# Performance work log

Hardware: AMD Instinct MI355X
Metric: run time of the kernel (lower is better)

## Reference

```python
import jax, jax.numpy as jnp
import numpy as np

B, S, D, H = 8, 1024, 1024, 16
HD = D // H  # head dim 64
NUM_REL = 7


def setup_inputs() -> dict:
    key = jax.random.key(0)
    ks = jax.random.split(key, 10)
    s = 0.02
    return {
        "hidden_states": jax.random.normal(ks[0], (B, S, D), dtype=jnp.float32),
        "attention_mask": jnp.zeros((B, 1, 1, S), dtype=jnp.float32),
        "relation": jax.random.randint(ks[1], (B, S, S), 0, NUM_REL, dtype=jnp.int32),
        "Wq": jax.random.normal(ks[2], (D, D), dtype=jnp.float32) * s,
        "bq": jnp.zeros((D,), dtype=jnp.float32),
        "Wk": jax.random.normal(ks[3], (D, D), dtype=jnp.float32) * s,
        "bk": jnp.zeros((D,), dtype=jnp.float32),
        "Wv": jax.random.normal(ks[4], (D, D), dtype=jnp.float32) * s,
        "bv": jnp.zeros((D,), dtype=jnp.float32),
        "rel_emb": jax.random.normal(ks[5], (NUM_REL, H), dtype=jnp.float32) * s,
    }


def reference(hidden_states, attention_mask, relation, Wq, bq, Wk, bk, Wv, bv, rel_emb):
    def heads(x):  # [B,S,D] -> [B,H,S,HD]
        return x.reshape(B, S, H, HD).transpose(0, 2, 1, 3)

    q = heads(hidden_states @ Wq.T + bq)
    k = heads(hidden_states @ Wk.T + bk)
    v = heads(hidden_states @ Wv.T + bv)

    scores = jnp.einsum("bhqd,bhkd->bhqk", q, k) / jnp.sqrt(jnp.float32(HD))
    # relation bias: gather [B,S,S,H] then move H to dim 1
    rel_bias = rel_emb[relation].transpose(0, 3, 1, 2)  # [B,H,S,S]
    scores = scores + rel_bias + attention_mask
    probs = jax.nn.softmax(scores, axis=-1)  # dropout is identity in eval
    ctx = jnp.einsum("bhqk,bhkd->bhqd", probs, v)
    return ctx.transpose(0, 2, 1, 3).reshape(B, S, D)
```

## Files before the change

kernel.cpp:

```cpp
#include <hip/hip_runtime.h>

#define NB 8
#define NS 1024
#define ND 1024
#define NH 16
#define NHD 64

typedef __attribute__((ext_vector_type(8))) short bf16x8;
typedef __attribute__((ext_vector_type(4))) float f32x4;
typedef __attribute__((ext_vector_type(4))) unsigned int u32x4;

#define GLOAD_LDS16(g, l) __builtin_amdgcn_global_load_lds(                    \
    (const __attribute__((address_space(1))) void*)(g),                        \
    (__attribute__((address_space(3))) void*)(l), 16, 0, 0)

static __device__ __forceinline__ unsigned short f2bf(float f) {
    unsigned int u = __builtin_bit_cast(unsigned int, f);
    unsigned int r = u + 0x7fffu + ((u >> 16) & 1u);
    return (unsigned short)(r >> 16);
}

static __device__ __forceinline__ unsigned int cvtpk(float lo, float hi) {
    unsigned int r;
    asm("v_cvt_pk_bf16_f32 %0, %1, %2" : "=v"(r) : "v"(lo), "v"(hi));
    return r;
}

static __device__ __forceinline__ float ldre(const float* t, unsigned int byteoff) {
    return *reinterpret_cast<const float*>(reinterpret_cast<const char*>(t) + byteoff);
}

__global__ void cvt_f32_bf16(const float* __restrict__ in, unsigned short* __restrict__ out, int n) {
    int i = (blockIdx.x * blockDim.x + threadIdx.x) * 4;
    if (i >= n) return;
    float4 v = *reinterpret_cast<const float4*>(in + i);
    ushort4 o;
    o.x = f2bf(v.x); o.y = f2bf(v.y); o.z = f2bf(v.z); o.w = f2bf(v.w);
    *reinterpret_cast<ushort4*>(out + i) = o;
}

__global__ void cvt_w3(const float* __restrict__ Wq, const float* __restrict__ Wk,
                       const float* __restrict__ Wv, unsigned short* __restrict__ out) {
    const float* src = (blockIdx.y == 0) ? Wq : (blockIdx.y == 1) ? Wk : Wv;
    int i = (blockIdx.x * blockDim.x + threadIdx.x) * 4;
    float4 v = *reinterpret_cast<const float4*>(src + i);
    ushort4 o;
    o.x = f2bf(v.x); o.y = f2bf(v.y); o.z = f2bf(v.z); o.w = f2bf(v.w);
    *reinterpret_cast<ushort4*>(out + (size_t)blockIdx.y * (ND * ND) + i) = o;
}

__global__ void pack_rel8(const int* __restrict__ rel, unsigned int* __restrict__ out) {
    int i = blockIdx.x * blockDim.x + threadIdx.x;
    int4 v = reinterpret_cast<const int4*>(rel)[i];
    out[i] = ((unsigned)v.x << 2) | ((unsigned)v.y << 10) |
             ((unsigned)v.z << 18) | ((unsigned)v.w << 26);
}

__global__ __launch_bounds__(256) void qkv_gemm(
    const unsigned short* __restrict__ A,
    const unsigned short* __restrict__ Wq, const unsigned short* __restrict__ Wk,
    const unsigned short* __restrict__ Wv,
    const float* __restrict__ bq, const float* __restrict__ bk, const float* __restrict__ bv,
    const float* __restrict__ mask,
    unsigned short* __restrict__ Qo, unsigned short* __restrict__ Ko, unsigned short* __restrict__ Vo)
{
    const int z = blockIdx.z;
    const unsigned short* W = (z == 0) ? Wq : (z == 1) ? Wk : Wv;
    const float* bias = (z == 0) ? bq : (z == 1) ? bk : bv;
    const int m0 = blockIdx.x * 128;
    const int n0 = blockIdx.y * 128;
    const float LOG2E = 1.4426950408889634f;
    const float QSCL = 0.125f * 1.4426950408889634f;

    __shared__ unsigned short As[128][64];
    __shared__ unsigned short Bs[128][64];

    const int tid = threadIdx.x;
    const int lane = tid & 63;
    const int wave = tid >> 6;
    const int wm = wave >> 1, wn = wave & 1;

    f32x4 acc[4][4] = {};

    const int crow = lane >> 3;
    const int gcol = ((lane & 7) ^ crow) * 8;
    const int kofs = (lane >> 4) * 8;

    for (int kb = 0; kb < ND; kb += 64) {
#pragma unroll
        for (int cc = 0; cc < 4; ++cc) {
            int c = wave * 4 + cc;
            GLOAD_LDS16(&A[(size_t)(m0 + c * 8 + crow) * ND + kb + gcol], &As[c * 8][0]);
            GLOAD_LDS16(&W[(size_t)(n0 + c * 8 + crow) * ND + kb + gcol], &Bs[c * 8][0]);
        }
        __syncthreads();
#pragma unroll
        for (int kk = 0; kk < 2; ++kk) {
            const int colx = (kk * 32 + kofs) ^ ((lane & 7) * 8);
            bf16x8 af[4], bfr[4];
#pragma unroll
            for (int i = 0; i < 4; ++i) {
                af[i]  = *reinterpret_cast<const bf16x8*>(&As[wm * 64 + i * 16 + (lane & 15)][colx]);
                bfr[i] = *reinterpret_cast<const bf16x8*>(&Bs[wn * 64 + i * 16 + (lane & 15)][colx]);
            }
#pragma unroll
            for (int mi = 0; mi < 4; ++mi)
#pragma unroll
                for (int ni = 0; ni < 4; ++ni)
                    acc[mi][ni] = __builtin_amdgcn_mfma_f32_16x16x32_bf16(af[mi], bfr[ni], acc[mi][ni], 0, 0, 0);
        }
        __syncthreads();
    }

#pragma unroll
    for (int ni = 0; ni < 4; ++ni) {
        int n = n0 + wn * 64 + ni * 16 + (lane & 15);
        float bv_ = bias[n];
        int h = n >> 6, hd = n & 63;
#pragma unroll
        for (int mi = 0; mi < 4; ++mi) {
            int m = m0 + wm * 64 + mi * 16 + (lane >> 4) * 4;
            int b = m >> 10, s = m & 1023;
            if (z == 2) {
                float4 mv = *reinterpret_cast<const float4*>(&mask[(size_t)b * NS + s]);
                ushort4 o;
                o.x = f2bf((acc[mi][ni][0] + bv_) * exp2f(mv.x * LOG2E));
                o.y = f2bf((acc[mi][ni][1] + bv_) * exp2f(mv.y * LOG2E));
                o.z = f2bf((acc[mi][ni][2] + bv_) * exp2f(mv.z * LOG2E));
                o.w = f2bf((acc[mi][ni][3] + bv_) * exp2f(mv.w * LOG2E));
                *reinterpret_cast<ushort4*>(&Vo[(((size_t)b * NH + h) * NHD + hd) * NS + s]) = o;
            } else if (z == 0) {
#pragma unroll
                for (int r2 = 0; r2 < 4; ++r2)
                    Qo[(((size_t)b * NH + h) * NS + s + r2) * NHD + hd] = f2bf((acc[mi][ni][r2] + bv_) * QSCL);
            } else {
#pragma unroll
                for (int r2 = 0; r2 < 4; ++r2)
                    Ko[(((size_t)b * NH + h) * NS + s + r2) * NHD + hd] = f2bf(acc[mi][ni][r2] + bv_);
            }
        }
    }
}

__global__ __launch_bounds__(512) void flash_attn(
    const unsigned short* __restrict__ Q, const unsigned short* __restrict__ Kb,
    const unsigned short* __restrict__ Vt,
    const unsigned char* __restrict__ rel8, const float* __restrict__ rel_emb,
    const float* __restrict__ mask, float* __restrict__ out)
{
    const int id = blockIdx.x;
    const int b = id & 7;
    const int h = (id >> 3) & 15;
    const int q0 = (id >> 7) * 128;
    const int tid = threadIdx.x, lane = tid & 63, wave = tid >> 6;
    const int g = lane >> 4, l15 = lane & 15;

    __shared__ unsigned short Ks[2][64][64];
    __shared__ unsigned short Vs[2][64][64];
    __shared__ unsigned short s_emask[NS];
    __shared__ float s_re2[8];
    const float LOG2E = 1.4426950408889634f;
    if (tid < 7) s_re2[tid] = rel_emb[tid * NH + h] * LOG2E - 4.0f;

    const unsigned short* Qh = Q  + (((size_t)b * NH + h) * NS) * NHD;
    const unsigned short* Kh = Kb + (((size_t)b * NH + h) * NS) * NHD;
    const unsigned short* Vh = Vt + (((size_t)b * NH + h) * NHD) * NS;
    const int qg = q0 + wave * 16 + l15;
    const unsigned char* __restrict__ relrow = rel8 + (size_t)b * NS * NS + (size_t)qg * NS;
    const float* __restrict__ maskb = mask + (size_t)b * NS;

    bf16x8 qa[2];
    qa[0] = *reinterpret_cast<const bf16x8*>(&Qh[(size_t)qg * NHD + g * 8]);
    qa[1] = *reinterpret_cast<const bf16x8*>(&Qh[(size_t)qg * NHD + 32 + g * 8]);

    f32x4 ctx[4] = {};
    f32x4 l_acc = {};
    float mofs = 0.f;
    bool everscaled = false;

    const int crow = lane >> 3;
    const int gcol = ((lane & 7) ^ crow) * 8;
    const int swz8 = (lane & 7) * 8;

    const int rho = wave * 8 + crow;
    const int kvperm = ((rho >> 5) << 5) + (((rho >> 2) & 3) << 3)
                     + (((rho >> 4) & 1) << 2) + (rho & 3);

#define STAGE(buf, kv)                                                                          \
    {                                                                                           \
        GLOAD_LDS16(&Kh[(size_t)((kv) + kvperm) * NHD + gcol], &Ks[buf][wave * 8][0]);          \
        GLOAD_LDS16(&Vh[(size_t)(wave * 8 + crow) * NS + (kv) + gcol], &Vs[buf][wave * 8][0]);  \
    }

#define LOADRM(S, t0)                                                                \
    {                                                                                \
        r##S##a = *reinterpret_cast<const uint2*>(&relrow[(t0) * 64 + 8 * g]);       \
        r##S##b = *reinterpret_cast<const uint2*>(&relrow[(t0) * 64 + 32 + 8 * g]);  \
    }

    uint2 rAa, rAb, rBa, rBb;

    STAGE(0, 0)
    LOADRM(A, 0)
    s_emask[tid] = f2bf(exp2f(maskb[tid] * LOG2E));
    s_emask[tid + 512] = f2bf(exp2f(maskb[tid + 512] * LOG2E));
    __syncthreads();

#define BODY(cur, S, SN, tc, tn)                                               \
  {                                                                            \
    if ((tn) < 16) {                                                           \
      STAGE(cur ^ 1, (tn) * 64)                                                \
      LOADRM(SN, tn)                                                           \
    }                                                                          \
    f32x4 sc[4] = {};                                                          \
    __builtin_amdgcn_s_setprio(1);                                             \
    _Pragma("unroll")                                                          \
    for (int kk = 0; kk < 2; ++kk) {                                           \
      const int colx = (kk * 32 + g * 8) ^ swz8;                               \
      _Pragma("unroll")                                                        \
      for (int tt = 0; tt < 4; ++tt) {                                         \
        bf16x8 kfrag = *reinterpret_cast<const bf16x8*>(&Ks[cur][tt * 16 + l15][colx]); \
        sc[tt] = __builtin_amdgcn_mfma_f32_16x16x32_bf16(kfrag, qa[kk], sc[tt], 0, 0, 0); \
      }                                                                        \
    }                                                                          \
    __builtin_amdgcn_s_setprio(0);                                             \
    const unsigned int rw[4] = {r##S##a.x, r##S##a.y, r##S##b.x, r##S##b.y};   \
    float pmax = -1e30f;                                                       \
    _Pragma("unroll")                                                          \
    for (int tt = 0; tt < 4; ++tt) {                                           \
      float v0 = sc[tt][0] + ldre(s_re2, rw[tt] & 0xFF);                       \
      float v1 = sc[tt][1] + ldre(s_re2, (rw[tt] >> 8) & 0xFF);                \
      float v2 = sc[tt][2] + ldre(s_re2, (rw[tt] >> 16) & 0xFF);               \
      float v3 = sc[tt][3] + ldre(s_re2, rw[tt] >> 24);                        \
      sc[tt][0] = v0; sc[tt][1] = v1; sc[tt][2] = v2; sc[tt][3] = v3;          \
      pmax = fmaxf(pmax, fmaxf(fmaxf(v0, v1), fmaxf(v2, v3)));                 \
    }                                                                          \
    if (!__all(pmax <= mofs + 8.0f)) {                                         \
      float pm = fmaxf(pmax, __shfl_xor(pmax, 16));                            \
      pm = fmaxf(pm, __shfl_xor(pm, 32));                                      \
      float mnew = fmaxf(mofs, pm);                                            \
      float alpha = exp2f(mofs - mnew);                                        \
      mofs = mnew;                                                             \
      everscaled = true;                                                       \
      float ar[4];                                                             \
      _Pragma("unroll")                                                        \
      for (int r = 0; r < 4; ++r) ar[r] = __shfl(alpha, 4 * g + r);            \
      _Pragma("unroll")                                                        \
      for (int r = 0; r < 4; ++r) l_acc[r] *= ar[r];                           \
      _Pragma("unroll")                                                        \
      for (int ht = 0; ht < 4; ++ht)                                           \
        _Pragma("unroll")                                                      \
        for (int r = 0; r < 4; ++r) ctx[ht][r] *= ar[r];                       \
    }                                                                          \
    unsigned int pw[8];                                                        \
    if (!everscaled) {                                                         \
      _Pragma("unroll")                                                        \
      for (int tt = 0; tt < 4; ++tt) {                                         \
        pw[2 * tt]     = cvtpk(exp2f(sc[tt][0]), exp2f(sc[tt][1]));            \
        pw[2 * tt + 1] = cvtpk(exp2f(sc[tt][2]), exp2f(sc[tt][3]));            \
      }                                                                        \
    } else {                                                                   \
      _Pragma("unroll")                                                        \
      for (int tt = 0; tt < 4; ++tt) {                                         \
        pw[2 * tt]     = cvtpk(exp2f(sc[tt][0] - mofs), exp2f(sc[tt][1] - mofs)); \
        pw[2 * tt + 1] = cvtpk(exp2f(sc[tt][2] - mofs), exp2f(sc[tt][3] - mofs)); \
      }                                                                        \
    }                                                                          \
    __builtin_amdgcn_s_setprio(1);                                             \
    _Pragma("unroll")                                                          \
    for (int kk = 0; kk < 2; ++kk) {                                           \
      u32x4 paw = {pw[4 * kk], pw[4 * kk + 1], pw[4 * kk + 2], pw[4 * kk + 3]};\
      bf16x8 pa = __builtin_bit_cast(bf16x8, paw);                             \
      const int colx = (kk * 32 + g * 8) ^ swz8;                               \
      bf16x8 mfr = *reinterpret_cast<const bf16x8*>(&s_emask[(tc) * 64 + kk * 32 + g * 8]); \
      l_acc = __builtin_amdgcn_mfma_f32_16x16x32_bf16(pa, mfr, l_acc, 0, 0, 0); \
      _Pragma("unroll")                                                        \
      for (int ht = 0; ht < 4; ++ht) {                                         \
        bf16x8 bfrag = *reinterpret_cast<const bf16x8*>(&Vs[cur][ht * 16 + l15][colx]); \
        ctx[ht] = __builtin_amdgcn_mfma_f32_16x16x32_bf16(pa, bfrag, ctx[ht], 0, 0, 0); \
      }                                                                        \
    }                                                                          \
    __builtin_amdgcn_s_setprio(0);                                             \
    __syncthreads();                                                           \
  }

    for (int t = 0; t < 16; t += 2) {
        BODY(0, A, B, t, t + 1)
        BODY(1, B, A, t + 1, t + 2)
    }
#undef BODY
#undef LOADRM
#undef STAGE

    float linv[4];
#pragma unroll
    for (int r = 0; r < 4; ++r) linv[r] = 1.0f / l_acc[r];
#pragma unroll
    for (int ht = 0; ht < 4; ++ht) {
        int hd = ht * 16 + l15;
#pragma unroll
        for (int r = 0; r < 4; ++r) {
            int qo = q0 + wave * 16 + 4 * g + r;
            out[((size_t)b * NS + qo) * ND + h * NHD + hd] = ctx[ht][r] * linv[r];
        }
    }
}

extern "C" void kernel_launch(void* const* d_in, const int* in_sizes, int n_in,
                              void* d_out, int out_size, void* d_ws, size_t ws_size,
                              hipStream_t stream) {
    const float* hs      = (const float*)d_in[0];
    const float* mask    = (const float*)d_in[1];
    const int*   rel     = (const int*)d_in[2];
    const float* Wq      = (const float*)d_in[3];
    const float* bq      = (const float*)d_in[4];
    const float* Wk      = (const float*)d_in[5];
    const float* bk      = (const float*)d_in[6];
    const float* Wv      = (const float*)d_in[7];
    const float* bv      = (const float*)d_in[8];
    const float* rel_emb = (const float*)d_in[9];
    float* out = (float*)d_out;

    char* ws = (char*)d_ws;
    unsigned short* q_bf  = (unsigned short*)(ws);
    unsigned short* k_bf  = (unsigned short*)(ws + ((size_t)16 << 20));
    unsigned short* vt_bf = (unsigned short*)(ws + ((size_t)32 << 20));
    unsigned short* hs_bf = (unsigned short*)(ws + ((size_t)48 << 20));
    unsigned short* w_bf  = (unsigned short*)(ws + ((size_t)64 << 20));
    unsigned char*  rel8  = (unsigned char*)(ws + ((size_t)48 << 20));

    const int nhs = NB * NS * ND;
    const int nw  = ND * ND;
    cvt_f32_bf16<<<nhs / 4 / 256, 256, 0, stream>>>(hs, hs_bf, nhs);
    cvt_w3<<<dim3(nw / 4 / 256, 3), 256, 0, stream>>>(Wq, Wk, Wv, w_bf);

    qkv_gemm<<<dim3((NB * NS) / 128, ND / 128, 3), 256, 0, stream>>>(
        hs_bf, w_bf, w_bf + (size_t)nw, w_bf + (size_t)2 * nw,
        bq, bk, bv, mask, q_bf, k_bf, vt_bf);

    pack_rel8<<<(NB * NS * NS / 4) / 256, 256, 0, stream>>>(rel, (unsigned int*)rel8);

    flash_attn<<<1024, 512, 0, stream>>>(
        q_bf, k_bf, vt_bf, rel8, rel_emb, mask, out);
}
```

Measured before the change: 163.9 us.

## Double-buffer QKV GEMM LDS tiles with K-step 32 to overlap loads and MFMA

Restructures the QKV projection GEMM main loop. Instead of a single 64-wide K tile, it uses two 32-wide LDS buffers and prefetches the next stage with async global-to-LDS loads while MFMAs run on the current one. This is meant to hide global load latency and cut to one barrier per step. It also changes the XOR swizzle to fit the narrower rows. In exchange there are twice as many iterations with half the MFMA work each, and the single barrier per step may not be enough to make the async LDS writes visible before use.

```diff
diff --git a/kernel.cpp b/kernel.cpp
--- a/kernel.cpp
+++ b/kernel.cpp
@@ -72,54 +72,59 @@
     const float LOG2E = 1.4426950408889634f;
     const float QSCL = 0.125f * 1.4426950408889634f;
 
-    __shared__ unsigned short As[128][64];
-    __shared__ unsigned short Bs[128][64];
+    __shared__ unsigned short As[2][128][32];
+    __shared__ unsigned short Bs[2][128][32];
 
     const int tid = threadIdx.x;
     const int lane = tid & 63;
     const int wave = tid >> 6;
     const int wm = wave >> 1, wn = wave & 1;
+    const int g = lane >> 4, l15 = lane & 15;
 
     f32x4 acc[4][4] = {};
 
-    const int crow = lane >> 3;
-    const int gcol = ((lane & 7) ^ crow) * 8;
-    const int kofs = (lane >> 4) * 8;
-
-    for (int kb = 0; kb < ND; kb += 64) {
-#pragma unroll
-        for (int cc = 0; cc < 4; ++cc) {
-            int c = wave * 4 + cc;
-            GLOAD_LDS16(&A[(size_t)(m0 + c * 8 + crow) * ND + kb + gcol], &As[c * 8][0]);
-            GLOAD_LDS16(&W[(size_t)(n0 + c * 8 + crow) * ND + kb + gcol], &Bs[c * 8][0]);
+    const int srow = lane >> 2;
+    const int scol = (((lane & 3) ^ (srow & 3)) << 3);
+    const int fcol = ((g ^ (l15 & 3)) << 3);
+
+#define GSTAGE(buf, kb)                                                                            \
+    {                                                                                              \
+        _Pragma("unroll")                                                                          \
+        for (int i = 0; i < 2; ++i) {                                                              \
+            int c = wave + i * 4;                                                                  \
+            GLOAD_LDS16(&A[(size_t)(m0 + c * 16 + srow) * ND + (kb) + scol], &As[buf][c * 16][0]); \
+            GLOAD_LDS16(&W[(size_t)(n0 + c * 16 + srow) * ND + (kb) + scol], &Bs[buf][c * 16][0]); \
+        }                                                                                          \
+    }
+
+    GSTAGE(0, 0)
+    __syncthreads();
+
+    for (int t = 0; t < 32; ++t) {
+        const int cur = t & 1;
+        if (t < 31) GSTAGE(cur ^ 1, (t + 1) * 32)
+        bf16x8 af[4], bfr[4];
+#pragma unroll
+        for (int i = 0; i < 4; ++i) {
+            af[i]  = *reinterpret_cast<const bf16x8*>(&As[cur][wm * 64 + i * 16 + l15][fcol]);
+            bfr[i] = *reinterpret_cast<const bf16x8*>(&Bs[cur][wn * 64 + i * 16 + l15][fcol]);
         }
+#pragma unroll
+        for (int mi = 0; mi < 4; ++mi)
+#pragma unroll
+            for (int ni = 0; ni < 4; ++ni)
+                acc[mi][ni] = __builtin_amdgcn_mfma_f32_16x16x32_bf16(af[mi], bfr[ni], acc[mi][ni], 0, 0, 0);
         __syncthreads();
-#pragma unroll
-        for (int kk = 0; kk < 2; ++kk) {
-            const int colx = (kk * 32 + kofs) ^ ((lane & 7) * 8);
-            bf16x8 af[4], bfr[4];
-#pragma unroll
-            for (int i = 0; i < 4; ++i) {
-                af[i]  = *reinterpret_cast<const bf16x8*>(&As[wm * 64 + i * 16 + (lane & 15)][colx]);
-                bfr[i] = *reinterpret_cast<const bf16x8*>(&Bs[wn * 64 + i * 16 + (lane & 15)][colx]);
-            }
-#pragma unroll
-            for (int mi = 0; mi < 4; ++mi)
-#pragma unroll
-                for (int ni = 0; ni < 4; ++ni)
-                    acc[mi][ni] = __builtin_amdgcn_mfma_f32_16x16x32_bf16(af[mi], bfr[ni], acc[mi][ni], 0, 0, 0);
-        }
-        __syncthreads();
     }
 
 #pragma unroll
     for (int ni = 0; ni < 4; ++ni) {
-        int n = n0 + wn * 64 + ni * 16 + (lane & 15);
+        int n = n0 + wn * 64 + ni * 16 + l15;
         float bv_ = bias[n];
         int h = n >> 6, hd = n & 63;
 #pragma unroll
         for (int mi = 0; mi < 4; ++mi) {
-            int m = m0 + wm * 64 + mi * 16 + (lane >> 4) * 4;
+            int m = m0 + wm * 64 + mi * 16 + g * 4;
             int b = m >> 10, s = m & 1023;
             if (z == 2) {
                 float4 mv = *reinterpret_cast<const float4*>(&mask[(size_t)b * NS + s]);
```

Measured after the change: 170.4 us. 4.0% more time.
